# Kernel optimization log

Hardware: AMD Instinct MI355X
Metric: run time of the kernel (lower is better)

## Reference

```python
import jax, jax.numpy as jnp
import numpy as np

EPS = 1e-12  # torch F.normalize eps


def _l2norm(v, axis):
    return v / jnp.maximum(jnp.linalg.norm(v, axis=axis, keepdims=True), EPS)


def setup_inputs() -> dict:
    key = jax.random.key(0)
    k1, k2, k3 = jax.random.split(key, 3)
    N, D, H, W, K = 32, 512, 64, 64, 64
    x = jax.random.normal(k1, (N, D, H, W), dtype=jnp.float32)
    conv_w = jax.random.normal(k2, (K, D), dtype=jnp.float32) * 0.05
    centroids = jax.random.normal(k3, (K, D), dtype=jnp.float32)
    return {"x": x, "conv_w": conv_w, "centroids": centroids}


def reference(x, conv_w, centroids):
    # x: [N, D, H, W]; conv_w: [K, D] (1x1 conv, no bias); centroids: [K, D]
    N, D, H, W = x.shape
    K = conv_w.shape[0]
    # descriptor-wise L2 normalization over channel dim
    x = _l2norm(x, axis=1)
    xf = x.reshape(N, D, H * W)                      # [N, D, P]
    # 1x1 conv == matmul over channels; softmax over clusters
    logits = jnp.einsum('kd,ndp->nkp', conv_w, xf)    # [N, K, P]
    a = jax.nn.softmax(logits, axis=1)                # [N, K, P]
    # vlad[n,k,d] = sum_p a[n,k,p] * (xf[n,d,p] - c[k,d])
    #            = (a @ xf^T)[n,k,d] - (sum_p a[n,k,p]) * c[k,d]
    vlad = jnp.einsum('nkp,ndp->nkd', a, xf) \
         - a.sum(axis=-1)[:, :, None] * centroids[None, :, :]  # [N, K, D]
    vlad = _l2norm(vlad, axis=2)                      # intra-normalization
    v = vlad.reshape(N, K * D)
    return _l2norm(v, axis=1)                         # global L2 norm
```

## Files before the change

kernel.cpp:

```cpp
#include <hip/hip_runtime.h>
#include <hip/hip_bf16.h>
#include <math.h>

#define Nn 32
#define Dd 512
#define Pp 4096
#define Kk 64
#define PSEG 4
static constexpr float EPSF = 1e-12f;

typedef short short8 __attribute__((ext_vector_type(8)));
typedef float floatx4 __attribute__((ext_vector_type(4)));

static __device__ __forceinline__ int f2b2(float a, float b) {
  __hip_bfloat162 h = __float22bfloat162_rn(float2{a, b});
  int r; __builtin_memcpy(&r, &h, 4); return r;
}
static __device__ __forceinline__ short8 pack8(const float* v) {
  union { short8 s; int i[4]; } u;
  u.i[0] = f2b2(v[0], v[1]); u.i[1] = f2b2(v[2], v[3]);
  u.i[2] = f2b2(v[4], v[5]); u.i[3] = f2b2(v[6], v[7]);
  return u.s;
}
static __device__ __forceinline__ short f2b1(float f) {
  unsigned u = __float_as_uint(f);
  return (short)((u + 0x7FFFu + ((u >> 16) & 1u)) >> 16);
}
static __device__ __forceinline__ float b2f(short s) {
  return __uint_as_float(((unsigned)(unsigned short)s) << 16);
}

__global__ __launch_bounds__(256) void k_assign(
    const float* __restrict__ x, const float* __restrict__ w,
    short* __restrict__ a_s, float* __restrict__ asum)
{
  __shared__ float xs[32][136];
  __shared__ short wf[2048];
  __shared__ float invs[128];

  const int tid = threadIdx.x;
  const int n  = blockIdx.x >> 5;
  const int p0 = (blockIdx.x & 31) * 128;
  const int wave = tid >> 6, lane = tid & 63;
  const int q = lane >> 4, pc = lane & 15;
  const int wp = wave * 32;

  const int dr = tid >> 3, fc = tid & 7;
  const int wk = tid >> 2, wq = tid & 3;

  floatx4 acc[4][2];
#pragma unroll
  for (int t = 0; t < 4; ++t)
#pragma unroll
    for (int s = 0; s < 2; ++s) acc[t][s] = floatx4{0.f, 0.f, 0.f, 0.f};
  float s16[16];
#pragma unroll
  for (int e = 0; e < 16; ++e) s16[e] = 0.f;

  const float* xrowb = x + (size_t)n * Dd * Pp + p0 + fc * 16;

  for (int dc = 0; dc < Dd; dc += 32) {
    {
      const float* wr = w + wk * Dd + dc + wq * 8;
      float wv[8];
      *(float4*)&wv[0] = *(const float4*)wr;
      *(float4*)&wv[4] = *(const float4*)(wr + 4);
      *(short8*)&wf[(wk * 4 + wq) * 8] = pack8(wv);
    }
    {
      const float* xr = xrowb + (size_t)(dc + dr) * Pp;
#pragma unroll
      for (int j = 0; j < 4; ++j) {
        float4 v = *(const float4*)(xr + j * 4);
        s16[j * 4 + 0] += v.x * v.x; s16[j * 4 + 1] += v.y * v.y;
        s16[j * 4 + 2] += v.z * v.z; s16[j * 4 + 3] += v.w * v.w;
        *(float4*)&xs[dr][fc * 16 + j * 4] = v;
      }
    }
    __syncthreads();
    short8 af[4];
#pragma unroll
    for (int t = 0; t < 4; ++t)
      af[t] = *(short8*)&wf[((t * 16 + pc) * 4 + q) * 8];
    short8 bf[2];
#pragma unroll
    for (int s = 0; s < 2; ++s) {
      float bv[8];
#pragma unroll
      for (int i = 0; i < 8; ++i) bv[i] = xs[q * 8 + i][wp + s * 16 + pc];
      bf[s] = pack8(bv);
    }
#pragma unroll
    for (int t = 0; t < 4; ++t)
#pragma unroll
      for (int s = 0; s < 2; ++s)
        acc[t][s] = __builtin_amdgcn_mfma_f32_16x16x32_bf16(af[t], bf[s], acc[t][s], 0, 0, 0);
    __syncthreads();
  }

  float* ssqp = &xs[0][0];
#pragma unroll
  for (int e = 0; e < 16; ++e) ssqp[e * 256 + tid] = s16[e];
  __syncthreads();
  if (tid < 128) {
    const int e = tid & 15, f = tid >> 4;
    float s = 0.f;
#pragma unroll
    for (int d2 = 0; d2 < 32; ++d2) s += ssqp[e * 256 + d2 * 8 + f];
    invs[tid] = 1.f / fmaxf(sqrtf(s), EPSF);
  }
  __syncthreads();

  float iv[2] = { invs[wp + pc], invs[wp + 16 + pc] };
  float mx[2] = { -1e30f, -1e30f };
#pragma unroll
  for (int t = 0; t < 4; ++t)
#pragma unroll
    for (int s = 0; s < 2; ++s)
#pragma unroll
      for (int r = 0; r < 4; ++r) {
        float l = acc[t][s][r] * iv[s];
        acc[t][s][r] = l;
        mx[s] = fmaxf(mx[s], l);
      }
#pragma unroll
  for (int s = 0; s < 2; ++s) {
    mx[s] = fmaxf(mx[s], __shfl_xor(mx[s], 16));
    mx[s] = fmaxf(mx[s], __shfl_xor(mx[s], 32));
  }
  float sm[2] = { 0.f, 0.f };
#pragma unroll
  for (int t = 0; t < 4; ++t)
#pragma unroll
    for (int s = 0; s < 2; ++s)
#pragma unroll
      for (int r = 0; r < 4; ++r) {
        float e = __expf(acc[t][s][r] - mx[s]);
        acc[t][s][r] = e;
        sm[s] += e;
      }
#pragma unroll
  for (int s = 0; s < 2; ++s) {
    sm[s] += __shfl_xor(sm[s], 16);
    sm[s] += __shfl_xor(sm[s], 32);
    sm[s] = 1.f / sm[s];
  }

  short* ab = (short*)&xs[0][0] + wave * 2048;
#pragma unroll
  for (int t = 0; t < 4; ++t)
#pragma unroll
    for (int s = 0; s < 2; ++s)
#pragma unroll
      for (int r = 0; r < 4; ++r)
        ab[(t * 16 + q * 4 + r) * 32 + s * 16 + pc] = f2b1(acc[t][s][r] * sm[s]);

#pragma unroll
  for (int pass = 0; pass < 4; ++pass) {
    int kr = pass * 16 + (lane >> 2);
    int c8 = (lane & 3) * 8;
    short8 av = *(short8*)&ab[kr * 32 + c8];
    float aw[8]; float s8 = 0.f;
#pragma unroll
    for (int i = 0; i < 8; ++i) { aw[i] = b2f(av[i]); s8 += aw[i]; }
    s8 += __shfl_down(s8, 1);
    s8 += __shfl_down(s8, 2);
    if ((lane & 3) == 0) atomicAdd(&asum[n * Kk + kr], s8);
    float ivv[8];
    *(float4*)&ivv[0] = *(const float4*)&invs[wp + c8];
    *(float4*)&ivv[4] = *(const float4*)&invs[wp + c8 + 4];
    float ov[8];
#pragma unroll
    for (int i = 0; i < 8; ++i) ov[i] = aw[i] * ivv[i];
    *(short8*)(a_s + ((size_t)(n * Kk + kr)) * Pp + p0 + wp + c8) = pack8(ov);
  }
}

__global__ __launch_bounds__(256) void k_vlad(
    const float* __restrict__ x, const short* __restrict__ a_s,
    float* __restrict__ vpart)
{
  const int tid = threadIdx.x;
  const int ps = blockIdx.x & 3;
  const int dt = (blockIdx.x >> 2) & 3;
  const int n  = blockIdx.x >> 4;
  const int wave = tid >> 6, lane = tid & 63;
  const int q = lane >> 4, pc = lane & 15;
  const int dw = dt * 128 + wave * 32;
  const int pb = ps * (Pp / PSEG);

  floatx4 acc[4][2];
#pragma unroll
  for (int t = 0; t < 4; ++t)
#pragma unroll
    for (int s = 0; s < 2; ++s) acc[t][s] = floatx4{0.f, 0.f, 0.f, 0.f};

  const short* ab0 = a_s + ((size_t)(n * Kk + pc)) * Pp + q * 8;
  const float* xb0 = x + ((size_t)(n * Dd + dw + pc)) * Pp + q * 8;

#pragma unroll 2
  for (int p = pb; p < pb + Pp / PSEG; p += 32) {
    short8 af[4];
#pragma unroll
    for (int t = 0; t < 4; ++t)
      af[t] = *(const short8*)(ab0 + (size_t)t * 16 * Pp + p);
    short8 bf[2];
#pragma unroll
    for (int s = 0; s < 2; ++s) {
      const float* xp = xb0 + (size_t)s * 16 * Pp + p;
      float bv[8];
      *(float4*)&bv[0] = *(const float4*)xp;
      *(float4*)&bv[4] = *(const float4*)(xp + 4);
      bf[s] = pack8(bv);
    }
#pragma unroll
    for (int t = 0; t < 4; ++t)
#pragma unroll
      for (int s = 0; s < 2; ++s)
        acc[t][s] = __builtin_amdgcn_mfma_f32_16x16x32_bf16(af[t], bf[s], acc[t][s], 0, 0, 0);
  }

  float* vb = vpart + (((size_t)ps * Nn + n) * Kk) * Dd;
#pragma unroll
  for (int t = 0; t < 4; ++t)
#pragma unroll
    for (int s = 0; s < 2; ++s)
#pragma unroll
      for (int r = 0; r < 4; ++r)
        vb[(size_t)(t * 16 + q * 4 + r) * Dd + dw + s * 16 + pc] = acc[t][s][r];
}

__global__ __launch_bounds__(128) void k_intra(
    const float* __restrict__ vpart, const float* __restrict__ asum,
    const float* __restrict__ cent, float* __restrict__ out, float* __restrict__ gnsq)
{
  __shared__ float red[2];
  const int nk = blockIdx.x;
  const int n = nk >> 6, k = nk & 63;
  const int tid = threadIdx.x;
  const int d = tid * 4;

  float4 v = {0.f, 0.f, 0.f, 0.f};
#pragma unroll
  for (int ps = 0; ps < PSEG; ++ps) {
    float4 t = *(const float4*)&vpart[(((size_t)ps * Nn + n) * Kk + k) * Dd + d];
    v.x += t.x; v.y += t.y; v.z += t.z; v.w += t.w;
  }
  float s = asum[n * Kk + k];
  float4 c = *(const float4*)&cent[(size_t)k * Dd + d];
  v.x -= s * c.x; v.y -= s * c.y; v.z -= s * c.z; v.w -= s * c.w;

  float qq = v.x * v.x + v.y * v.y + v.z * v.z + v.w * v.w;
#pragma unroll
  for (int off = 32; off; off >>= 1) qq += __shfl_down(qq, off);
  if ((tid & 63) == 0) red[tid >> 6] = qq;
  __syncthreads();
  float norm = sqrtf(red[0] + red[1]);
  float r = 1.f / fmaxf(norm, EPSF);
  v.x *= r; v.y *= r; v.z *= r; v.w *= r;
  *(float4*)&out[(size_t)n * (Kk * Dd) + (size_t)k * Dd + d] = v;
  if (tid == 0) {
    float t = norm * r;
    atomicAdd(&gnsq[n], t * t);
  }
}

__global__ __launch_bounds__(256) void k_gscale(
    float* __restrict__ out, const float* __restrict__ gnsq)
{
  size_t i = ((size_t)blockIdx.x * 256 + threadIdx.x) * 4;
  int n = (int)(i >> 15);
  float r = 1.f / fmaxf(sqrtf(gnsq[n]), EPSF);
  float4 v = *(float4*)&out[i];
  v.x *= r; v.y *= r; v.z *= r; v.w *= r;
  *(float4*)&out[i] = v;
}

extern "C" void kernel_launch(void* const* d_in, const int* in_sizes, int n_in,
                              void* d_out, int out_size, void* d_ws, size_t ws_size,
                              hipStream_t stream) {
  (void)in_sizes; (void)n_in; (void)out_size; (void)ws_size;
  const float* x    = (const float*)d_in[0];
  const float* w    = (const float*)d_in[1];
  const float* cent = (const float*)d_in[2];
  float* out = (float*)d_out;

  short* a_s   = (short*)d_ws;
  float* asum  = (float*)(a_s + (size_t)Nn * Kk * Pp);
  float* gnsq  = asum + Nn * Kk;
  float* vpart = gnsq + 64;

  hipMemsetAsync(asum, 0, (Nn * Kk + 64) * sizeof(float), stream);
  k_assign<<<Nn * 32, 256, 0, stream>>>(x, w, a_s, asum);
  k_vlad<<<Nn * 4 * PSEG, 256, 0, stream>>>(x, a_s, vpart);
  k_intra<<<Nn * Kk, 128, 0, stream>>>(vpart, asum, cent, out, gnsq);
  k_gscale<<<(Nn * Kk * Dd) / (256 * 4), 256, 0, stream>>>(out, gnsq);
}
```

Before: 452.1 us.

## Prepack conv weights to bf16 and load x directly into MFMA fragments

A new small kernel converts conv weights into a bf16 fragment-ordered buffer once per call. k_assign now loads x straight from global memory into registers in MFMA operand layout, with x as the A operand and weights as B. This drops the shared-memory staging and both __syncthreads per D-chunk, and the per-pixel norm and softmax are done with cross-lane shuffles. In exchange the x reads become 4-byte strided per lane rather than float4 vectors, which may hurt coalescing, and there is one extra tiny launch.

```diff
diff --git a/kernel.cpp b/kernel.cpp
--- a/kernel.cpp
+++ b/kernel.cpp
@@ -30,12 +30,27 @@
   return __uint_as_float(((unsigned)(unsigned short)s) << 16);
 }
 
+__global__ __launch_bounds__(256) void k_wpack(
+    const float* __restrict__ w, short* __restrict__ wp)
+{
+  int id = blockIdx.x * 256 + threadIdx.x;
+  int chunk = id >> 6, k = id & 63;
+  const float* src = w + (size_t)k * Dd + chunk * 32;
+  short* dst = wp + ((size_t)(chunk * 64 + k)) * 32;
+#pragma unroll
+  for (int q = 0; q < 4; ++q) {
+    float v[8];
+    *(float4*)&v[0] = *(const float4*)(src + q * 8);
+    *(float4*)&v[4] = *(const float4*)(src + q * 8 + 4);
+    *(short8*)(dst + q * 8) = pack8(v);
+  }
+}
+
 __global__ __launch_bounds__(256) void k_assign(
-    const float* __restrict__ x, const float* __restrict__ w,
+    const float* __restrict__ x, const short* __restrict__ wp,
     short* __restrict__ a_s, float* __restrict__ asum)
 {
-  __shared__ float xs[32][136];
-  __shared__ short wf[2048];
+  __shared__ short ab4[4][2048];
   __shared__ float invs[128];
 
   const int tid = threadIdx.x;
@@ -43,123 +58,86 @@
   const int p0 = (blockIdx.x & 31) * 128;
   const int wave = tid >> 6, lane = tid & 63;
   const int q = lane >> 4, pc = lane & 15;
-  const int wp = wave * 32;
-
-  const int dr = tid >> 3, fc = tid & 7;
-  const int wk = tid >> 2, wq = tid & 3;
+  const int wpx = wave * 32;
 
   floatx4 acc[4][2];
 #pragma unroll
   for (int t = 0; t < 4; ++t)
 #pragma unroll
     for (int s = 0; s < 2; ++s) acc[t][s] = floatx4{0.f, 0.f, 0.f, 0.f};
-  float s16[16];
-#pragma unroll
-  for (int e = 0; e < 16; ++e) s16[e] = 0.f;
-
-  const float* xrowb = x + (size_t)n * Dd * Pp + p0 + fc * 16;
+  float sq[2] = {0.f, 0.f};
+
+  const float* xa0 = x + (size_t)n * Dd * Pp + (size_t)(q * 8) * Pp + p0 + wpx + pc;
+  const float* xa1 = xa0 + 16;
 
   for (int dc = 0; dc < Dd; dc += 32) {
-    {
-      const float* wr = w + wk * Dd + dc + wq * 8;
-      float wv[8];
-      *(float4*)&wv[0] = *(const float4*)wr;
-      *(float4*)&wv[4] = *(const float4*)(wr + 4);
-      *(short8*)&wf[(wk * 4 + wq) * 8] = pack8(wv);
-    }
-    {
-      const float* xr = xrowb + (size_t)(dc + dr) * Pp;
-#pragma unroll
-      for (int j = 0; j < 4; ++j) {
-        float4 v = *(const float4*)(xr + j * 4);
-        s16[j * 4 + 0] += v.x * v.x; s16[j * 4 + 1] += v.y * v.y;
-        s16[j * 4 + 2] += v.z * v.z; s16[j * 4 + 3] += v.w * v.w;
-        *(float4*)&xs[dr][fc * 16 + j * 4] = v;
-      }
-    }
-    __syncthreads();
-    short8 af[4];
+    short8 bf[4];
+    const short* wc = wp + (size_t)(dc >> 5) * 2048 + pc * 32 + q * 8;
 #pragma unroll
     for (int t = 0; t < 4; ++t)
-      af[t] = *(short8*)&wf[((t * 16 + pc) * 4 + q) * 8];
-    short8 bf[2];
-#pragma unroll
-    for (int s = 0; s < 2; ++s) {
-      float bv[8];
-#pragma unroll
-      for (int i = 0; i < 8; ++i) bv[i] = xs[q * 8 + i][wp + s * 16 + pc];
-      bf[s] = pack8(bv);
-    }
-#pragma unroll
-    for (int t = 0; t < 4; ++t)
-#pragma unroll
-      for (int s = 0; s < 2; ++s)
-        acc[t][s] = __builtin_amdgcn_mfma_f32_16x16x32_bf16(af[t], bf[s], acc[t][s], 0, 0, 0);
-    __syncthreads();
-  }
-
-  float* ssqp = &xs[0][0];
-#pragma unroll
-  for (int e = 0; e < 16; ++e) ssqp[e * 256 + tid] = s16[e];
-  __syncthreads();
-  if (tid < 128) {
-    const int e = tid & 15, f = tid >> 4;
-    float s = 0.f;
-#pragma unroll
-    for (int d2 = 0; d2 < 32; ++d2) s += ssqp[e * 256 + d2 * 8 + f];
-    invs[tid] = 1.f / fmaxf(sqrtf(s), EPSF);
-  }
-  __syncthreads();
-
-  float iv[2] = { invs[wp + pc], invs[wp + 16 + pc] };
-  float mx[2] = { -1e30f, -1e30f };
-#pragma unroll
-  for (int t = 0; t < 4; ++t)
-#pragma unroll
-    for (int s = 0; s < 2; ++s)
-#pragma unroll
-      for (int r = 0; r < 4; ++r) {
-        float l = acc[t][s][r] * iv[s];
-        acc[t][s][r] = l;
-        mx[s] = fmaxf(mx[s], l);
-      }
+      bf[t] = *(const short8*)(wc + t * 512);
+    float v0[8], v1[8];
+#pragma unroll
+    for (int j = 0; j < 8; ++j) {
+      float a0 = xa0[(size_t)j * Pp];
+      float a1 = xa1[(size_t)j * Pp];
+      v0[j] = a0; v1[j] = a1;
+      sq[0] += a0 * a0; sq[1] += a1 * a1;
+    }
+    short8 af0 = pack8(v0), af1 = pack8(v1);
+#pragma unroll
+    for (int t = 0; t < 4; ++t) {
+      acc[t][0] = __builtin_amdgcn_mfma_f32_16x16x32_bf16(af0, bf[t], acc[t][0], 0, 0, 0);
+      acc[t][1] = __builtin_amdgcn_mfma_f32_16x16x32_bf16(af1, bf[t], acc[t][1], 0, 0, 0);
+    }
+    xa0 += (size_t)32 * Pp; xa1 += (size_t)32 * Pp;
+  }
+
 #pragma unroll
   for (int s = 0; s < 2; ++s) {
-    mx[s] = fmaxf(mx[s], __shfl_xor(mx[s], 16));
-    mx[s] = fmaxf(mx[s], __shfl_xor(mx[s], 32));
-  }
-  float sm[2] = { 0.f, 0.f };
-#pragma unroll
-  for (int t = 0; t < 4; ++t)
-#pragma unroll
-    for (int s = 0; s < 2; ++s)
-#pragma unroll
-      for (int r = 0; r < 4; ++r) {
-        float e = __expf(acc[t][s][r] - mx[s]);
-        acc[t][s][r] = e;
-        sm[s] += e;
-      }
-#pragma unroll
-  for (int s = 0; s < 2; ++s) {
-    sm[s] += __shfl_xor(sm[s], 16);
-    sm[s] += __shfl_xor(sm[s], 32);
-    sm[s] = 1.f / sm[s];
-  }
-
-  short* ab = (short*)&xs[0][0] + wave * 2048;
-#pragma unroll
-  for (int t = 0; t < 4; ++t)
-#pragma unroll
-    for (int s = 0; s < 2; ++s)
-#pragma unroll
-      for (int r = 0; r < 4; ++r)
-        ab[(t * 16 + q * 4 + r) * 32 + s * 16 + pc] = f2b1(acc[t][s][r] * sm[s]);
+    float t = sq[s];
+    t += __shfl_xor(t, 16);
+    t += __shfl_xor(t, 32);
+    if (q == 0) invs[wpx + s * 16 + pc] = 1.f / fmaxf(sqrtf(t), EPSF);
+  }
+  float ivr[2][4];
+#pragma unroll
+  for (int s = 0; s < 2; ++s)
+#pragma unroll
+    for (int r = 0; r < 4; ++r)
+      ivr[s][r] = invs[wpx + s * 16 + q * 4 + r];
+
+#pragma unroll
+  for (int s = 0; s < 2; ++s)
+#pragma unroll
+    for (int r = 0; r < 4; ++r) {
+      float l[4];
+#pragma unroll
+      for (int t = 0; t < 4; ++t) l[t] = acc[t][s][r] * ivr[s][r];
+      float mx = fmaxf(fmaxf(l[0], l[1]), fmaxf(l[2], l[3]));
+      mx = fmaxf(mx, __shfl_xor(mx, 1));
+      mx = fmaxf(mx, __shfl_xor(mx, 2));
+      mx = fmaxf(mx, __shfl_xor(mx, 4));
+      mx = fmaxf(mx, __shfl_xor(mx, 8));
+      float e[4], sm = 0.f;
+#pragma unroll
+      for (int t = 0; t < 4; ++t) { e[t] = __expf(l[t] - mx); sm += e[t]; }
+      sm += __shfl_xor(sm, 1);
+      sm += __shfl_xor(sm, 2);
+      sm += __shfl_xor(sm, 4);
+      sm += __shfl_xor(sm, 8);
+      float si = 1.f / sm;
+      int pl = s * 16 + q * 4 + r;
+#pragma unroll
+      for (int t = 0; t < 4; ++t)
+        ab4[wave][(t * 16 + pc) * 32 + pl] = f2b1(e[t] * si);
+    }
 
 #pragma unroll
   for (int pass = 0; pass < 4; ++pass) {
     int kr = pass * 16 + (lane >> 2);
     int c8 = (lane & 3) * 8;
-    short8 av = *(short8*)&ab[kr * 32 + c8];
+    short8 av = *(short8*)&ab4[wave][kr * 32 + c8];
     float aw[8]; float s8 = 0.f;
 #pragma unroll
     for (int i = 0; i < 8; ++i) { aw[i] = b2f(av[i]); s8 += aw[i]; }
@@ -167,12 +145,12 @@
     s8 += __shfl_down(s8, 2);
     if ((lane & 3) == 0) atomicAdd(&asum[n * Kk + kr], s8);
     float ivv[8];
-    *(float4*)&ivv[0] = *(const float4*)&invs[wp + c8];
-    *(float4*)&ivv[4] = *(const float4*)&invs[wp + c8 + 4];
+    *(float4*)&ivv[0] = *(const float4*)&invs[wpx + c8];
+    *(float4*)&ivv[4] = *(const float4*)&invs[wpx + c8 + 4];
     float ov[8];
 #pragma unroll
     for (int i = 0; i < 8; ++i) ov[i] = aw[i] * ivv[i];
-    *(short8*)(a_s + ((size_t)(n * Kk + kr)) * Pp + p0 + wp + c8) = pack8(ov);
+    *(short8*)(a_s + ((size_t)(n * Kk + kr)) * Pp + p0 + wpx + c8) = pack8(ov);
   }
 }
 
@@ -289,9 +267,11 @@
   float* asum  = (float*)(a_s + (size_t)Nn * Kk * Pp);
   float* gnsq  = asum + Nn * Kk;
   float* vpart = gnsq + 64;
+  short* wpk   = (short*)(vpart + (size_t)PSEG * Nn * Kk * Dd);
 
   hipMemsetAsync(asum, 0, (Nn * Kk + 64) * sizeof(float), stream);
-  k_assign<<<Nn * 32, 256, 0, stream>>>(x, w, a_s, asum);
+  k_wpack<<<4, 256, 0, stream>>>(w, wpk);
+  k_assign<<<Nn * 32, 256, 0, stream>>>(x, wpk, a_s, asum);
   k_vlad<<<Nn * 4 * PSEG, 256, 0, stream>>>(x, a_s, vpart);
   k_intra<<<Nn * Kk, 128, 0, stream>>>(vpart, asum, cent, out, gnsq);
   k_gscale<<<(Nn * Kk * Dd) / (256 * 4), 256, 0, stream>>>(out, gnsq);
```

Measured after the change: 464.7 us. 2.8% more time.
